# Optimization experiments

Measured on AMD Instinct MI355X. Metric: run time of the kernel, lower is better.

Reference implementation:

```python
import jax, jax.numpy as jnp
import numpy as np

N_HEAD = 16
N_EMBD = 1024
BLOCK = 2048
B, T = 4, 2048


def setup_inputs() -> dict:
    key = jax.random.key(0)
    ks = jax.random.split(key, 5)
    s = 0.02
    return {
        "x": jax.random.normal(ks[0], (B, T, N_EMBD), dtype=jnp.float32),
        "qkv_w": jax.random.normal(ks[1], (3 * N_EMBD, N_EMBD), dtype=jnp.float32) * s,
        "qkv_b": jnp.zeros((3 * N_EMBD,), dtype=jnp.float32),
        "proj_w": jax.random.normal(ks[2], (N_EMBD, N_EMBD), dtype=jnp.float32) * s,
        "proj_b": jnp.zeros((N_EMBD,), dtype=jnp.float32),
    }


def reference(x, qkv_w, qkv_b, proj_w, proj_b):
    Bx, Tx, C = x.shape
    hd = C // N_HEAD
    qkv = x @ qkv_w.T + qkv_b  # [B,T,3C]
    q, k, v = jnp.split(qkv, 3, axis=-1)
    # [B,T,C] -> [B,H,T,hd]
    def heads(t):
        return t.reshape(Bx, Tx, N_HEAD, hd).transpose(0, 2, 1, 3)
    q, k, v = heads(q), heads(k), heads(v)
    scores = jnp.einsum("bhqd,bhkd->bhqk", q, k) / jnp.sqrt(jnp.float32(hd))
    causal = jnp.tril(jnp.ones((Tx, Tx), dtype=bool))
    scores = jnp.where(causal[None, None, :, :], scores, -jnp.inf)
    attn = jax.nn.softmax(scores, axis=-1)
    out = jnp.einsum("bhqk,bhkd->bhqd", attn, v)
    out = out.transpose(0, 2, 1, 3).reshape(Bx, Tx, C)
    return out @ proj_w.T + proj_b
```

## Files before the change

### kernel.cpp

```cpp
#include <hip/hip_runtime.h>
#include <stdint.h>
#include <math.h>

#define DEVI __device__ __forceinline__

typedef __attribute__((ext_vector_type(8))) short bf16x8;
typedef __attribute__((ext_vector_type(4))) float f32x4;

DEVI unsigned short f2bf(float f) {
  union { float f; unsigned u; } v; v.f = f;
  unsigned u = v.u;
  u += 0x7fffu + ((u >> 16) & 1u);
  return (unsigned short)(u >> 16);
}

DEVI unsigned cvt_pk_bf16(float a, float b) {
  unsigned r;
  asm("v_cvt_pk_bf16_f32 %0, %1, %2" : "=v"(r) : "v"(a), "v"(b));
  return r;
}

DEVI f32x4 mfma16(bf16x8 a, bf16x8 b, f32x4 c) {
  return __builtin_amdgcn_mfma_f32_16x16x32_bf16(a, b, c, 0, 0, 0);
}

DEVI void gld16(const unsigned short* g, unsigned short* l) {
  __builtin_amdgcn_global_load_lds(
      (const __attribute__((address_space(1))) unsigned int*)(uintptr_t)g,
      (__attribute__((address_space(3))) unsigned int*)(unsigned int)(uintptr_t)l,
      16, 0, 0);
}

#define VMCNT(n) asm volatile("s_waitcnt vmcnt(" #n ")" ::: "memory")
#define BAR()                              \
  do {                                     \
    __builtin_amdgcn_s_barrier();          \
    __builtin_amdgcn_sched_barrier(0);     \
  } while (0)

__global__ __launch_bounds__(256) void cvt_kernel(const float* __restrict__ in,
                                                  unsigned short* __restrict__ out, int n) {
  int i = (blockIdx.x * 256 + threadIdx.x) * 4;
  if (i < n) {
    float4 v = *(const float4*)(in + i);
    unsigned lo = f2bf(v.x) | ((unsigned)f2bf(v.y) << 16);
    unsigned hi = f2bf(v.z) | ((unsigned)f2bf(v.w) << 16);
    uint2 o; o.x = lo; o.y = hi;
    *(uint2*)(out + i) = o;
  }
}

template <int MODE>
__global__ __launch_bounds__(512, 2) void gemm8(
    const unsigned short* __restrict__ A, const unsigned short* __restrict__ Bw,
    const float* __restrict__ bias, float* __restrict__ Cf,
    unsigned short* __restrict__ Qo, unsigned short* __restrict__ Ko,
    unsigned short* __restrict__ Vo, int M, int N, int K, int nbx) {
  extern __shared__ unsigned short lds[];
  const int tid = threadIdx.x;
  const int lane = tid & 63;
  const int w = tid >> 6;
  const int wm = w >> 2, wn = w & 3;
  const int lr = lane & 15, lq = lane >> 4;

  const int cpx = gridDim.x >> 3;
  const int swz = (blockIdx.x & 7) * cpx + (blockIdx.x >> 3);
  const int bx = swz % nbx, by = swz / nbx;
  const int m0 = by * 256, n0 = bx * 256;

  const int sr = lane >> 3;
  const int sc = ((lane & 7) ^ sr) << 3;
  const unsigned short* pa = A + (size_t)(m0 + sr) * K + sc;
  const unsigned short* pb = Bw + (size_t)(n0 + sr) * K + sc;

  const int aA0 = w, aA1 = 16 + w;
  const int aB0 = 8 + w, aB1 = 24 + w;
  const int bA0 = (w & 3) + ((w >> 2) << 3), bA1 = bA0 + 16;
  const int bB0 = bA0 + 4, bB1 = bA1 + 4;

  const int bs0 = (lq ^ (lr & 7)) << 3;
  const int bs1 = ((lq + 4) ^ (lr & 7)) << 3;

  f32x4 acc[8][4] = {};

  auto sA = [&](int buf, int kt, int c) {
    gld16(pa + (size_t)(c << 3) * K + kt, lds + buf * 32768 + (c << 9));
  };
  auto sB = [&](int buf, int kt, int c) {
    gld16(pb + (size_t)(c << 3) * K + kt, lds + buf * 32768 + 16384 + (c << 9));
  };

#define PH(buf, mh, nh)                                                          \
  {                                                                              \
    const unsigned short* As_ = lds + (buf) * 32768;                             \
    const unsigned short* Bs_ = As_ + 16384;                                     \
    bf16x8 a0[4], a1[4], b0[2], b1[2];                                           \
    _Pragma("unroll") for (int i = 0; i < 4; ++i) {                              \
      int ar = wm * 128 + (mh) * 64 + i * 16 + lr;                               \
      a0[i] = *(const bf16x8*)(As_ + ar * 64 + bs0);                             \
      a1[i] = *(const bf16x8*)(As_ + ar * 64 + bs1);                             \
    }                                                                            \
    _Pragma("unroll") for (int j = 0; j < 2; ++j) {                              \
      int br = wn * 64 + (nh) * 32 + j * 16 + lr;                                \
      b0[j] = *(const bf16x8*)(Bs_ + br * 64 + bs0);                             \
      b1[j] = *(const bf16x8*)(Bs_ + br * 64 + bs1);                             \
    }                                                                            \
    __builtin_amdgcn_s_setprio(1);                                               \
    _Pragma("unroll") for (int i = 0; i < 4; ++i)                                \
      _Pragma("unroll") for (int j = 0; j < 2; ++j) {                            \
        acc[(mh) * 4 + i][(nh) * 2 + j] =                                        \
            mfma16(a0[i], b0[j], acc[(mh) * 4 + i][(nh) * 2 + j]);               \
        acc[(mh) * 4 + i][(nh) * 2 + j] =                                        \
            mfma16(a1[i], b1[j], acc[(mh) * 4 + i][(nh) * 2 + j]);               \
      }                                                                          \
    __builtin_amdgcn_s_setprio(0);                                               \
  }

  sA(0, 0, aA0); sA(0, 0, aA1);
  sB(0, 0, bA0); sB(0, 0, bA1);
  sB(0, 0, bB0); sB(0, 0, bB1);
  sA(0, 0, aB0); sA(0, 0, aB1);
  VMCNT(4);
  BAR();

  const int NT = K >> 6;
  for (int t = 0; t < NT - 1; ++t) {
    const int buf = t & 1, nb = buf ^ 1;
    const int kt = (t + 1) << 6;
    sA(nb, kt, aA0); sA(nb, kt, aA1);
    PH(buf, 0, 0);
    VMCNT(4); BAR();
    sB(nb, kt, bA0); sB(nb, kt, bA1);
    PH(buf, 0, 1);
    VMCNT(4); BAR();
    sB(nb, kt, bB0); sB(nb, kt, bB1);
    PH(buf, 1, 0);
    sA(nb, kt, aB0); sA(nb, kt, aB1);
    PH(buf, 1, 1);
    VMCNT(4); BAR();
  }
  {
    const int buf = (NT - 1) & 1;
    PH(buf, 0, 0);
    VMCNT(2); BAR();
    PH(buf, 0, 1);
    VMCNT(0); BAR();
    PH(buf, 1, 0);
    PH(buf, 1, 1);
  }
#undef PH

#pragma unroll
  for (int mt = 0; mt < 8; ++mt) {
#pragma unroll
    for (int nt = 0; nt < 4; ++nt) {
      int n_g = n0 + wn * 64 + nt * 16 + lr;
      float bv = bias[n_g];
#pragma unroll
      for (int r = 0; r < 4; ++r) {
        int m_g = m0 + wm * 128 + mt * 16 + lq * 4 + r;
        float v = acc[mt][nt][r] + bv;
        if (MODE == 1) {
          Cf[(size_t)m_g * N + n_g] = v;
        } else {
          int which = n_g >> 10;
          int rem = n_g & 1023;
          int h = rem >> 6, d = rem & 63;
          int b = m_g >> 11, tt = m_g & 2047;
          size_t idx = (((size_t)(b * 16 + h) * 2048) + tt) * 64 + d;
          unsigned short* p = (which == 0) ? Qo : ((which == 1) ? Ko : Vo);
          p[idx] = f2bf(v);
        }
      }
    }
  }
}

__global__ __launch_bounds__(512, 4) void attn_kernel(
    const unsigned short* __restrict__ Q, const unsigned short* __restrict__ K,
    const unsigned short* __restrict__ V, unsigned short* __restrict__ Y) {
  constexpr int T = 2048, HD = 64, H = 16;
  __shared__ unsigned short Kt[2][64 * 72];
  __shared__ unsigned short Vt[2][64 * 72];
  __shared__ unsigned short Pt[8][16 * 72];

  const int tid = threadIdx.x;
  const int lane = tid & 63;
  const int w = tid >> 6;
  const int lr = lane & 15, lq = lane >> 4;
  const int pair = blockIdx.x;
  const int h = blockIdx.y;
  const int b = blockIdx.z;
  const size_t bh = (size_t)(b * H + h) * T * HD;
  const float SC = 0.125f * 1.44269504089f;

  const int krow = tid >> 3, kcb = (tid & 7) << 3;
  const int vrow = lane, vc = w << 3;

  float4 kr, vr;
  auto load_tile = [&](int jt) {
    const int c0 = jt * 64;
    kr = *(const float4*)(K + bh + (size_t)(c0 + krow) * HD + kcb);
    vr = *(const float4*)(V + bh + (size_t)(c0 + vrow) * HD + vc);
  };
  auto stage = [&](int buf) {
    *(float4*)(&Kt[buf][krow * 72 + kcb]) = kr;
    const unsigned short* vp = (const unsigned short*)&vr;
#pragma unroll
    for (int j = 0; j < 8; ++j) Vt[buf][(vc + j) * 72 + vrow] = vp[j];
  };

  load_tile(0);

  for (int phase = 0; phase < 2; ++phase) {
    const int qt = phase ? (15 - pair) : pair;
    const int q0 = qt * 128;
    const int nkv = 2 * qt + 2;
    const int qmin = q0 + w * 16;
    const int qmax = qmin + 15;

    bf16x8 qf[2];
#pragma unroll
    for (int kb = 0; kb < 2; ++kb)
      qf[kb] = *(const bf16x8*)(Q + bh + (size_t)(qmin + lr) * HD + kb * 32 + lq * 8);

    f32x4 o[4] = {};
    float mi = -INFINITY, li = 0.f;

    stage(0);
    load_tile(1);
    __syncthreads();

    for (int jt = 0; jt < nkv; ++jt) {
      const int c0 = jt * 64;
      const int buf = jt & 1;

      if (c0 <= qmax) {
        f32x4 s[4];
#pragma unroll
        for (int nt = 0; nt < 4; ++nt) {
          bf16x8 kf0 = *(const bf16x8*)(&Kt[buf][(nt * 16 + lr) * 72 + lq * 8]);
          bf16x8 kf1 = *(const bf16x8*)(&Kt[buf][(nt * 16 + lr) * 72 + 32 + lq * 8]);
          f32x4 z = {};
          z = mfma16(kf0, qf[0], z);
          s[nt] = mfma16(kf1, qf[1], z);
        }
        if (c0 + 63 > qmin) {
          int qg = qmin + lr;
#pragma unroll
          for (int nt = 0; nt < 4; ++nt)
#pragma unroll
            for (int r = 0; r < 4; ++r) {
              int kvg = c0 + nt * 16 + lq * 4 + r;
              s[nt][r] = (kvg > qg) ? -INFINITY : s[nt][r] * SC;
            }
        } else {
#pragma unroll
          for (int nt = 0; nt < 4; ++nt)
#pragma unroll
            for (int r = 0; r < 4; ++r) s[nt][r] *= SC;
        }
        float mx = -INFINITY;
#pragma unroll
        for (int nt = 0; nt < 4; ++nt)
          mx = fmaxf(mx, fmaxf(fmaxf(s[nt][0], s[nt][1]),
                               fmaxf(s[nt][2], s[nt][3])));
        mx = fmaxf(mx, __shfl_xor(mx, 16));
        mx = fmaxf(mx, __shfl_xor(mx, 32));
        float mnew = fmaxf(mi, mx);
        float alpha = __builtin_amdgcn_exp2f(mi - mnew);
        mi = mnew;
        float rs = 0.f;
#pragma unroll
        for (int nt = 0; nt < 4; ++nt) {
          float p0 = __builtin_amdgcn_exp2f(s[nt][0] - mnew);
          float p1 = __builtin_amdgcn_exp2f(s[nt][1] - mnew);
          float p2 = __builtin_amdgcn_exp2f(s[nt][2] - mnew);
          float p3 = __builtin_amdgcn_exp2f(s[nt][3] - mnew);
          rs += (p0 + p1) + (p2 + p3);
          uint2 pk;
          pk.x = cvt_pk_bf16(p0, p1);
          pk.y = cvt_pk_bf16(p2, p3);
          *(uint2*)(&Pt[w][lr * 72 + nt * 16 + lq * 4]) = pk;
        }
        rs += __shfl_xor(rs, 16);
        rs += __shfl_xor(rs, 32);
        li = li * alpha + rs;
#pragma unroll
        for (int nt = 0; nt < 4; ++nt)
#pragma unroll
          for (int r = 0; r < 4; ++r) o[nt][r] *= alpha;
        bf16x8 pf[2];
#pragma unroll
        for (int kb = 0; kb < 2; ++kb)
          pf[kb] = *(const bf16x8*)(&Pt[w][lr * 72 + kb * 32 + lq * 8]);
#pragma unroll
        for (int nt = 0; nt < 4; ++nt) {
          bf16x8 vf0 = *(const bf16x8*)(&Vt[buf][(nt * 16 + lr) * 72 + lq * 8]);
          bf16x8 vf1 = *(const bf16x8*)(&Vt[buf][(nt * 16 + lr) * 72 + 32 + lq * 8]);
          o[nt] = mfma16(vf0, pf[0], o[nt]);
          o[nt] = mfma16(vf1, pf[1], o[nt]);
        }
      }

      if (jt + 1 < nkv) {
        stage(buf ^ 1);
        if (jt + 2 < nkv) load_tile(jt + 2);
        else if (phase == 0) load_tile(0);
        __syncthreads();
      }
    }

    {
      float inv = 1.f / li;
      int t_g = qmin + lr;
#pragma unroll
      for (int nt = 0; nt < 4; ++nt) {
        uint2 yv;
        yv.x = cvt_pk_bf16(o[nt][0] * inv, o[nt][1] * inv);
        yv.y = cvt_pk_bf16(o[nt][2] * inv, o[nt][3] * inv);
        *(uint2*)(Y + ((size_t)(b * T + t_g)) * 1024 + h * 64 + nt * 16 + lq * 4) = yv;
      }
    }
  }
}

extern "C" void kernel_launch(void* const* d_in, const int* in_sizes, int n_in,
                              void* d_out, int out_size, void* d_ws, size_t ws_size,
                              hipStream_t stream) {
  const float* x = (const float*)d_in[0];
  const float* qkv_w = (const float*)d_in[1];
  const float* qkv_b = (const float*)d_in[2];
  const float* proj_w = (const float*)d_in[3];
  const float* proj_b = (const float*)d_in[4];
  float* out = (float*)d_out;

  unsigned short* ws = (unsigned short*)d_ws;
  unsigned short* xb = ws;
  unsigned short* wqkv = xb + 8388608;
  unsigned short* wproj = wqkv + 3145728;
  unsigned short* Qb = wproj + 1048576;
  unsigned short* Kb = Qb + 8388608;
  unsigned short* Vb = Kb + 8388608;
  unsigned short* Yb = Vb + 8388608;

  auto* g0 = gemm8<0>;
  auto* g1 = gemm8<1>;
  static bool attr_set = false;
  if (!attr_set) {
    (void)hipFuncSetAttribute((const void*)g0,
                              hipFuncAttributeMaxDynamicSharedMemorySize, 131072);
    (void)hipFuncSetAttribute((const void*)g1,
                              hipFuncAttributeMaxDynamicSharedMemorySize, 131072);
    attr_set = true;
  }

  cvt_kernel<<<8388608 / 1024, 256, 0, stream>>>(x, xb, 8388608);
  cvt_kernel<<<3145728 / 1024, 256, 0, stream>>>(qkv_w, wqkv, 3145728);
  cvt_kernel<<<1048576 / 1024, 256, 0, stream>>>(proj_w, wproj, 1048576);

  gemm8<0><<<dim3(384), 512, 131072, stream>>>(xb, wqkv, qkv_b, nullptr, Qb, Kb, Vb,
                                               8192, 3072, 1024, 12);
  attn_kernel<<<dim3(8, 16, 4), 512, 0, stream>>>(Qb, Kb, Vb, Yb);
  gemm8<1><<<dim3(128), 512, 131072, stream>>>(Yb, wproj, proj_b, out, nullptr, nullptr,
                                               nullptr, 8192, 1024, 1024, 4);
}
```

Before: 261.4 us.

## Store V transposed from QKV GEMM, add lazy softmax rescale and MFMA priority

The QKV GEMM epilogue now writes V in a transposed [b,h,d,t] layout with packed bf16 stores. This lets the attention kernel load V tiles with a single vectorized LDS store instead of eight scalar transposing writes. In the attention loop, the scale multiply is folded into an fma inside exp2, and the running max and output are rescaled only when a new max exceeds the old one by more than 8. The row-sum shuffle reduction is deferred to the end, and the MFMA sections are wrapped in s_setprio. The thresholded rescale lets probabilities reach up to 2^8 before renormalization, which carries some bf16 and overflow risk.

```diff
diff --git a/kernel.cpp b/kernel.cpp
--- a/kernel.cpp
+++ b/kernel.cpp
@@ -156,20 +156,30 @@
     for (int nt = 0; nt < 4; ++nt) {
       int n_g = n0 + wn * 64 + nt * 16 + lr;
       float bv = bias[n_g];
-#pragma unroll
-      for (int r = 0; r < 4; ++r) {
-        int m_g = m0 + wm * 128 + mt * 16 + lq * 4 + r;
-        float v = acc[mt][nt][r] + bv;
-        if (MODE == 1) {
-          Cf[(size_t)m_g * N + n_g] = v;
+      if (MODE == 1) {
+#pragma unroll
+        for (int r = 0; r < 4; ++r) {
+          int m_g = m0 + wm * 128 + mt * 16 + lq * 4 + r;
+          Cf[(size_t)m_g * N + n_g] = acc[mt][nt][r] + bv;
+        }
+      } else {
+        int which = n_g >> 10;
+        int rem = n_g & 1023;
+        int h = rem >> 6, d = rem & 63;
+        int m_base = m0 + wm * 128 + mt * 16 + lq * 4;
+        int b = m_base >> 11, tt = m_base & 2047;
+        if (which == 2) {
+          uint2 pv;
+          pv.x = cvt_pk_bf16(acc[mt][nt][0] + bv, acc[mt][nt][1] + bv);
+          pv.y = cvt_pk_bf16(acc[mt][nt][2] + bv, acc[mt][nt][3] + bv);
+          *(uint2*)(Vo + (((size_t)(b * 16 + h) * 64 + d) * 2048 + tt)) = pv;
         } else {
-          int which = n_g >> 10;
-          int rem = n_g & 1023;
-          int h = rem >> 6, d = rem & 63;
-          int b = m_g >> 11, tt = m_g & 2047;
-          size_t idx = (((size_t)(b * 16 + h) * 2048) + tt) * 64 + d;
-          unsigned short* p = (which == 0) ? Qo : ((which == 1) ? Ko : Vo);
-          p[idx] = f2bf(v);
+          unsigned short* p = (which == 0) ? Qo : Ko;
+#pragma unroll
+          for (int r = 0; r < 4; ++r) {
+            size_t idx = (((size_t)(b * 16 + h) * 2048) + tt + r) * 64 + d;
+            p[idx] = f2bf(acc[mt][nt][r] + bv);
+          }
         }
       }
     }
@@ -195,19 +205,16 @@
   const float SC = 0.125f * 1.44269504089f;
 
   const int krow = tid >> 3, kcb = (tid & 7) << 3;
-  const int vrow = lane, vc = w << 3;
 
   float4 kr, vr;
   auto load_tile = [&](int jt) {
     const int c0 = jt * 64;
     kr = *(const float4*)(K + bh + (size_t)(c0 + krow) * HD + kcb);
-    vr = *(const float4*)(V + bh + (size_t)(c0 + vrow) * HD + vc);
+    vr = *(const float4*)(V + bh + (size_t)krow * T + c0 + kcb);
   };
   auto stage = [&](int buf) {
     *(float4*)(&Kt[buf][krow * 72 + kcb]) = kr;
-    const unsigned short* vp = (const unsigned short*)&vr;
-#pragma unroll
-    for (int j = 0; j < 8; ++j) Vt[buf][(vc + j) * 72 + vrow] = vp[j];
+    *(float4*)(&Vt[buf][krow * 72 + kcb]) = vr;
   };
 
   load_tile(0);
@@ -237,6 +244,7 @@
 
       if (c0 <= qmax) {
         f32x4 s[4];
+        __builtin_amdgcn_s_setprio(1);
 #pragma unroll
         for (int nt = 0; nt < 4; ++nt) {
           bf16x8 kf0 = *(const bf16x8*)(&Kt[buf][(nt * 16 + lr) * 72 + lq * 8]);
@@ -245,6 +253,7 @@
           z = mfma16(kf0, qf[0], z);
           s[nt] = mfma16(kf1, qf[1], z);
         }
+        __builtin_amdgcn_s_setprio(0);
         if (c0 + 63 > qmin) {
           int qg = qmin + lr;
 #pragma unroll
@@ -252,13 +261,8 @@
 #pragma unroll
             for (int r = 0; r < 4; ++r) {
               int kvg = c0 + nt * 16 + lq * 4 + r;
-              s[nt][r] = (kvg > qg) ? -INFINITY : s[nt][r] * SC;
+              if (kvg > qg) s[nt][r] = -INFINITY;
             }
-        } else {
-#pragma unroll
-          for (int nt = 0; nt < 4; ++nt)
-#pragma unroll
-            for (int r = 0; r < 4; ++r) s[nt][r] *= SC;
         }
         float mx = -INFINITY;
 #pragma unroll
@@ -267,33 +271,36 @@
                                fmaxf(s[nt][2], s[nt][3])));
         mx = fmaxf(mx, __shfl_xor(mx, 16));
         mx = fmaxf(mx, __shfl_xor(mx, 32));
-        float mnew = fmaxf(mi, mx);
-        float alpha = __builtin_amdgcn_exp2f(mi - mnew);
-        mi = mnew;
+        float mxs = mx * SC;
+        if (!__all(mxs <= mi + 8.f)) {
+          float mnew = fmaxf(mi, mxs);
+          float alpha = __builtin_amdgcn_exp2f(mi - mnew);
+          mi = mnew;
+          li *= alpha;
+#pragma unroll
+          for (int nt = 0; nt < 4; ++nt)
+#pragma unroll
+            for (int r = 0; r < 4; ++r) o[nt][r] *= alpha;
+        }
         float rs = 0.f;
 #pragma unroll
         for (int nt = 0; nt < 4; ++nt) {
-          float p0 = __builtin_amdgcn_exp2f(s[nt][0] - mnew);
-          float p1 = __builtin_amdgcn_exp2f(s[nt][1] - mnew);
-          float p2 = __builtin_amdgcn_exp2f(s[nt][2] - mnew);
-          float p3 = __builtin_amdgcn_exp2f(s[nt][3] - mnew);
+          float p0 = __builtin_amdgcn_exp2f(fmaf(s[nt][0], SC, -mi));
+          float p1 = __builtin_amdgcn_exp2f(fmaf(s[nt][1], SC, -mi));
+          float p2 = __builtin_amdgcn_exp2f(fmaf(s[nt][2], SC, -mi));
+          float p3 = __builtin_amdgcn_exp2f(fmaf(s[nt][3], SC, -mi));
           rs += (p0 + p1) + (p2 + p3);
           uint2 pk;
           pk.x = cvt_pk_bf16(p0, p1);
           pk.y = cvt_pk_bf16(p2, p3);
           *(uint2*)(&Pt[w][lr * 72 + nt * 16 + lq * 4]) = pk;
         }
-        rs += __shfl_xor(rs, 16);
-        rs += __shfl_xor(rs, 32);
-        li = li * alpha + rs;
-#pragma unroll
-        for (int nt = 0; nt < 4; ++nt)
-#pragma unroll
-          for (int r = 0; r < 4; ++r) o[nt][r] *= alpha;
+        li += rs;
         bf16x8 pf[2];
 #pragma unroll
         for (int kb = 0; kb < 2; ++kb)
           pf[kb] = *(const bf16x8*)(&Pt[w][lr * 72 + kb * 32 + lq * 8]);
+        __builtin_amdgcn_s_setprio(1);
 #pragma unroll
         for (int nt = 0; nt < 4; ++nt) {
           bf16x8 vf0 = *(const bf16x8*)(&Vt[buf][(nt * 16 + lr) * 72 + lq * 8]);
@@ -301,6 +308,7 @@
           o[nt] = mfma16(vf0, pf[0], o[nt]);
           o[nt] = mfma16(vf1, pf[1], o[nt]);
         }
+        __builtin_amdgcn_s_setprio(0);
       }
 
       if (jt + 1 < nkv) {
@@ -312,6 +320,8 @@
     }
 
     {
+      li += __shfl_xor(li, 16);
+      li += __shfl_xor(li, 32);
       float inv = 1.f / li;
       int t_g = qmin + lr;
 #pragma unroll
```

Result: no change. 257.6 us (-1.4%).
